# Kernel tuning notes

Measured on AMD Instinct MI355X. Metric: run time of the kernel, lower is better.

## Reference

```python
import jax, jax.numpy as jnp
import numpy as np


def floor_ste(x):
    # forward: floor(x); backward: identity (straight-through estimator)
    return x + jax.lax.stop_gradient(jnp.floor(x) - x)


def _int_polynomial(x_int, sf):
    c0, c1, c2 = 0.35815147, 0.96963238, 1.0
    b_int = floor_ste((c1 / c0) / sf)
    c_int = floor_ste((c2 / c0) / (sf * sf))
    z = x_int * (x_int + b_int) + c_int
    return z, c0 * sf * sf


def _int_exp(x_int, sf):
    x0 = -0.69314718
    n = 15
    x0_int = floor_ste(x0 / sf)
    x_int = jnp.maximum(x_int, n * x0_int)
    q = floor_ste(x_int / x0_int)
    r = x_int - x0_int * q
    exp_int, exp_sf = _int_polynomial(r, sf)
    exp_int = jnp.maximum(floor_ste(exp_int * jnp.exp2(n - q)), 0.0)
    return exp_int, exp_sf / (2.0 ** n)


def _int_softmax(x, sf):
    x_int = x / sf
    x_int = x_int - jnp.max(x_int, axis=-1, keepdims=True)
    exp_int, exp_sf = _int_exp(x_int, sf)
    exp_int_sum = jnp.sum(exp_int, axis=-1, keepdims=True)
    return exp_int, exp_int_sum, exp_sf


def setup_inputs() -> dict:
    key = jax.random.key(0)
    k1, = jax.random.split(key, 1)
    x = jax.random.normal(k1, (2, 16, 1024, 1024), dtype=jnp.float32)
    scale = jnp.float32(0.05)          # activation quantization step
    threshold = jnp.array([0.1], dtype=jnp.float32)  # nn.Parameter init
    return {"x": x, "scale": scale, "threshold": threshold}


def reference(x, scale, threshold):
    output_bit = 8
    threshold_bits = 8
    exp_int, exp_int_sum, exp_sf = _int_softmax(x, scale)
    factor = floor_ste((2.0 ** 32) / exp_int_sum)
    out_scale_A = threshold / (2.0 ** output_bit - 1.0)   # shape [1]
    out_scale_B = 1.0 / (2.0 ** output_bit - 1.0)
    approx_threshold = (floor_ste(threshold * 2.0 ** threshold_bits)
                        * exp_int_sum / (2.0 ** threshold_bits))
    mask_A = exp_int <= approx_threshold
    exp_int_A = jnp.where(mask_A, exp_int, 0.0)
    exp_int_B = jnp.where(mask_A, 0.0, exp_int)
    softmax_int_A = floor_ste(exp_int_A * factor / ((2.0 ** 32) * out_scale_A))
    softmax_int_B = floor_ste(exp_int_B * factor / ((2.0 ** 32) * out_scale_B))
    softmax_int_B = jnp.minimum(softmax_int_B, 255.0)
    return softmax_int_A * out_scale_A + softmax_int_B * out_scale_B
```

## Files before the change

### kernel.cpp

```cpp
#include <hip/hip_runtime.h>
#include <math.h>

#pragma clang fp contract(off)

#define TPB 256
#define ROWLEN 1024

typedef float f32x4 __attribute__((ext_vector_type(4)));

static __device__ __forceinline__ float bcast_f32(float v) {
    return __int_as_float(__builtin_amdgcn_readfirstlane(__float_as_int(v)));
}

__device__ __forceinline__ float wave_max_dpp(float m) {
    const int NI = 0xff800000;
    int v;
    v = __builtin_amdgcn_update_dpp(NI, __float_as_int(m), 0x111, 0xf, 0xf, false);
    m = fmaxf(m, __int_as_float(v));
    v = __builtin_amdgcn_update_dpp(NI, __float_as_int(m), 0x112, 0xf, 0xf, false);
    m = fmaxf(m, __int_as_float(v));
    v = __builtin_amdgcn_update_dpp(NI, __float_as_int(m), 0x114, 0xf, 0xf, false);
    m = fmaxf(m, __int_as_float(v));
    v = __builtin_amdgcn_update_dpp(NI, __float_as_int(m), 0x118, 0xf, 0xf, false);
    m = fmaxf(m, __int_as_float(v));
    v = __builtin_amdgcn_update_dpp(NI, __float_as_int(m), 0x142, 0xa, 0xf, false);
    m = fmaxf(m, __int_as_float(v));
    v = __builtin_amdgcn_update_dpp(NI, __float_as_int(m), 0x143, 0xc, 0xf, false);
    m = fmaxf(m, __int_as_float(v));
    return __int_as_float(__builtin_amdgcn_readlane(__float_as_int(m), 63));
}

__device__ __forceinline__ void wave_sum_dpp2(unsigned& a, unsigned& b) {
    int v0, v1;
#define SSTG(sel, rm, bm) \
    v0 = __builtin_amdgcn_update_dpp(0, (int)a, sel, rm, bm, false); \
    v1 = __builtin_amdgcn_update_dpp(0, (int)b, sel, rm, bm, false); \
    a += (unsigned)v0; b += (unsigned)v1;
    SSTG(0x111,0xf,0xf) SSTG(0x112,0xf,0xf) SSTG(0x114,0xf,0xf)
    SSTG(0x118,0xf,0xf) SSTG(0x142,0xa,0xf) SSTG(0x143,0xc,0xf)
#undef SSTG
    a = (unsigned)__builtin_amdgcn_readlane((int)a, 63);
    b = (unsigned)__builtin_amdgcn_readlane((int)b, 63);
}

__device__ __forceinline__ float fac_exact(double s) {
    const float r0 = __builtin_amdgcn_rcpf((float)s);
    float qf = floorf(4294967296.0f * r0);
    const double t = (double)qf * s;
    if (t > 4294967296.0)           qf -= 1.0f;
    else if (t + s <= 4294967296.0) qf += 1.0f;
    return qf;
}

__global__ __launch_bounds__(TPB, 8) void qsplit_int_softmax_kernel(
    const float* __restrict__ x,
    const float* __restrict__ scale_p,
    const float* __restrict__ thr_p,
    float* __restrict__ out,
    const int rows)
{
    const int tid  = threadIdx.x;
    const int lane = tid & 63;
    const int wid  = tid >> 6;
    const int r    = (int)(blockIdx.x << 2) | wid;
    if (r >= rows) return;

    const float sf  = scale_p[0];
    const float thr = thr_p[0];

    const float rh = bcast_f32(1.0f / sf);
    const float er = __builtin_fmaf(-sf, rh, 1.0f);
    const float rl = bcast_f32(rh * er);

    #define DF_DIV(a) ({ float _p = (a) * rh; \
                         float _e = __builtin_fmaf((a), rh, -_p); \
                         _p + __builtin_fmaf((a), rl, _e); })
    const float x0f    = bcast_f32(floorf(DF_DIV(-0.69314718f)));
    const float bfc    = bcast_f32(floorf(DF_DIV(2.7073824f)));
    const float s2     = sf * sf;
    const float r2h    = 1.0f / s2;
    const float r2e    = __builtin_fmaf(-s2, r2h, 1.0f);
    const float r2l    = r2h * r2e;
    const float cq     = __builtin_fmaf(2.7921141f, r2l,
                         2.7921141f * r2h);
    const float cfc    = bcast_f32(floorf(cq));
    const float clampf = bcast_f32(15.0f * x0f);
    const float invx0f = bcast_f32(1.0f / x0f);

    const float osA  = bcast_f32(thr / 255.0f);
    const float osB  = bcast_f32(1.0f / 255.0f);
    const float invA = bcast_f32(1.0f / (4294967296.0f * osA));
    const float invB = bcast_f32(1.0f / (4294967296.0f * osB));
    const float thrq = bcast_f32(floorf(thr * 256.0f));

    const float* px = x + (size_t)r * ROWLEN + ((size_t)lane << 2);
    float a[16];
    #pragma unroll
    for (int g = 0; g < 4; ++g) {
        const f32x4 v = *(const f32x4*)(px + (g << 8));
        a[4*g+0] = v[0]; a[4*g+1] = v[1];
        a[4*g+2] = v[2]; a[4*g+3] = v[3];
    }

    #pragma unroll
    for (int j = 0; j < 16; ++j) {
        const float xx = a[j];
        const float p  = xx * rh;
        const float e  = __builtin_fmaf(xx, rh, -p);
        a[j] = p + __builtin_fmaf(xx, rl, e);
    }

    float t0 = fmaxf(a[0],a[1]),  t1 = fmaxf(a[2],a[3]);
    float t2 = fmaxf(a[4],a[5]),  t3 = fmaxf(a[6],a[7]);
    float t4 = fmaxf(a[8],a[9]),  t5 = fmaxf(a[10],a[11]);
    float t6 = fmaxf(a[12],a[13]),t7 = fmaxf(a[14],a[15]);
    t0 = fmaxf(t0,t1); t2 = fmaxf(t2,t3); t4 = fmaxf(t4,t5); t6 = fmaxf(t6,t7);
    const float m = wave_max_dpp(fmaxf(fmaxf(t0,t2), fmaxf(t4,t6)));

    unsigned usum = 0;
    #pragma unroll
    for (int j = 0; j < 16; ++j) {
        float v = a[j] - m;
        v = fmaxf(v, clampf);
        const float qf = floorf(v * invx0f);
        const int   qi = (int)qf;
        const float rr = v - x0f * qf;
        const float t  = rr + bfc;
        const float z  = rr * t + cfc;
        float ei = floorf(ldexpf(z, 15 - qi));
        ei = fmaxf(ei, 0.0f);
        a[j] = ei;
        usum += (unsigned)ei;
    }

    unsigned lo = usum & 0xFFFFu, hi = usum >> 16;
    wave_sum_dpp2(lo, hi);
    const double s = (double)(((unsigned long long)hi << 16) + lo);

    const float fac_f = bcast_f32(fac_exact(s));
    const float ath_f = bcast_f32((float)(((double)thrq * s) * (1.0 / 256.0)));

    float* po = out + (size_t)r * ROWLEN + ((size_t)lane << 2);
    #pragma unroll
    for (int g = 0; g < 4; ++g) {
        f32x4 o;
        #pragma unroll
        for (int jj = 0; jj < 4; ++jj) {
            const float ei  = a[4*g+jj];
            const bool  isA = (ei <= ath_f);
            const float t1_ = ei * fac_f;
            const float t2_ = t1_ * (isA ? invA : invB);
            float si = floorf(t2_);
            si = fminf(si, isA ? 3.0e38f : 255.0f);
            o[jj] = si * (isA ? osA : osB);
        }
        __builtin_nontemporal_store(o, (f32x4*)(po + (g << 8)));
    }
}

extern "C" void kernel_launch(void* const* d_in, const int* in_sizes, int n_in,
                              void* d_out, int out_size, void* d_ws, size_t ws_size,
                              hipStream_t stream) {
    const float* x     = (const float*)d_in[0];
    const float* scale = (const float*)d_in[1];
    const float* thr   = (const float*)d_in[2];
    float* out = (float*)d_out;

    const int total = in_sizes[0];
    const int rows  = total / ROWLEN;

    const int blocks = (rows + 3) / 4;

    qsplit_int_softmax_kernel<<<dim3(blocks), dim3(TPB), 0, stream>>>(
        x, scale, thr, out, rows);
}
```

Before: 233.8 us.

## Use persistent waves with LDS double-staging via global_load_lds prefetch

```diff
diff --git a/kernel.cpp b/kernel.cpp
--- a/kernel.cpp
+++ b/kernel.cpp
@@ -5,6 +5,7 @@
 
 #define TPB 256
 #define ROWLEN 1024
+#define BLOCKS 1024
 
 typedef float f32x4 __attribute__((ext_vector_type(4)));
 
@@ -52,7 +53,7 @@
     return qf;
 }
 
-__global__ __launch_bounds__(TPB, 8) void qsplit_int_softmax_kernel(
+__global__ __launch_bounds__(TPB) void qsplit_int_softmax_kernel(
     const float* __restrict__ x,
     const float* __restrict__ scale_p,
     const float* __restrict__ thr_p,
@@ -62,8 +63,15 @@
     const int tid  = threadIdx.x;
     const int lane = tid & 63;
     const int wid  = tid >> 6;
-    const int r    = (int)(blockIdx.x << 2) | wid;
-    if (r >= rows) return;
+
+    __shared__ float lds[4][ROWLEN];
+
+    const int gw = (int)(blockIdx.x << 2) | wid;
+    const int W  = (int)(gridDim.x << 2);
+    const int chunk = (rows + W - 1) / W;
+    int r          = gw * chunk;
+    const int rend = (r + chunk < rows) ? (r + chunk) : rows;
+    if (r >= rend) return;
 
     const float sf  = scale_p[0];
     const float thr = thr_p[0];
@@ -93,69 +101,93 @@
     const float invB = bcast_f32(1.0f / (4294967296.0f * osB));
     const float thrq = bcast_f32(floorf(thr * 256.0f));
 
-    const float* px = x + (size_t)r * ROWLEN + ((size_t)lane << 2);
-    float a[16];
-    #pragma unroll
-    for (int g = 0; g < 4; ++g) {
-        const f32x4 v = *(const f32x4*)(px + (g << 8));
-        a[4*g+0] = v[0]; a[4*g+1] = v[1];
-        a[4*g+2] = v[2]; a[4*g+3] = v[3];
+    #define STAGE(row) do { \
+        const float* _s = x + (size_t)(row) * ROWLEN + ((size_t)lane << 2); \
+        _Pragma("unroll") \
+        for (int _g = 0; _g < 4; ++_g) { \
+            __builtin_amdgcn_global_load_lds( \
+                (const __attribute__((address_space(1))) void*)(_s + (_g << 8)), \
+                (__attribute__((address_space(3))) void*)&lds[wid][_g << 8], \
+                16, 0, 0); \
+        } \
+    } while (0)
+
+    STAGE(r);
+
+    for (; r < rend; ++r) {
+        asm volatile("s_waitcnt vmcnt(0)" ::: "memory");
+
+        f32x4 w0 = *(const f32x4*)&lds[wid][(0 << 8) | (lane << 2)];
+        f32x4 w1 = *(const f32x4*)&lds[wid][(1 << 8) | (lane << 2)];
+        f32x4 w2 = *(const f32x4*)&lds[wid][(2 << 8) | (lane << 2)];
+        f32x4 w3 = *(const f32x4*)&lds[wid][(3 << 8) | (lane << 2)];
+
+        asm volatile("s_waitcnt lgkmcnt(0)" ::: "memory");
+
+        if (r + 1 < rend) STAGE(r + 1);
+
+        float a[16];
+        a[0]=w0[0]; a[1]=w0[1]; a[2]=w0[2]; a[3]=w0[3];
+        a[4]=w1[0]; a[5]=w1[1]; a[6]=w1[2]; a[7]=w1[3];
+        a[8]=w2[0]; a[9]=w2[1]; a[10]=w2[2]; a[11]=w2[3];
+        a[12]=w3[0]; a[13]=w3[1]; a[14]=w3[2]; a[15]=w3[3];
+
+        #pragma unroll
+        for (int j = 0; j < 16; ++j) {
+            const float xx = a[j];
+            const float p  = xx * rh;
+            const float e  = __builtin_fmaf(xx, rh, -p);
+            a[j] = p + __builtin_fmaf(xx, rl, e);
+        }
+
+        float t0 = fmaxf(a[0],a[1]),  t1 = fmaxf(a[2],a[3]);
+        float t2 = fmaxf(a[4],a[5]),  t3 = fmaxf(a[6],a[7]);
+        float t4 = fmaxf(a[8],a[9]),  t5 = fmaxf(a[10],a[11]);
+        float t6 = fmaxf(a[12],a[13]),t7 = fmaxf(a[14],a[15]);
+        t0 = fmaxf(t0,t1); t2 = fmaxf(t2,t3); t4 = fmaxf(t4,t5); t6 = fmaxf(t6,t7);
+        const float m = wave_max_dpp(fmaxf(fmaxf(t0,t2), fmaxf(t4,t6)));
+
+        unsigned usum = 0;
+        #pragma unroll
+        for (int j = 0; j < 16; ++j) {
+            float v = a[j] - m;
+            v = fmaxf(v, clampf);
+            const float qf = floorf(v * invx0f);
+            const int   qi = (int)qf;
+            const float rr = v - x0f * qf;
+            const float t  = rr + bfc;
+            const float z  = rr * t + cfc;
+            float ei = floorf(ldexpf(z, 15 - qi));
+            ei = fmaxf(ei, 0.0f);
+            a[j] = ei;
+            usum += (unsigned)ei;
+        }
+
+        unsigned lo = usum & 0xFFFFu, hi = usum >> 16;
+        wave_sum_dpp2(lo, hi);
+        const double s = (double)(((unsigned long long)hi << 16) + lo);
+
+        const float fac_f = bcast_f32(fac_exact(s));
+        const float ath_f = bcast_f32((float)(((double)thrq * s) * (1.0 / 256.0)));
+
+        float* po = out + (size_t)r * ROWLEN + ((size_t)lane << 2);
+        #pragma unroll
+        for (int g = 0; g < 4; ++g) {
+            f32x4 o;
+            #pragma unroll
+            for (int jj = 0; jj < 4; ++jj) {
+                const float ei  = a[4*g+jj];
+                const bool  isA = (ei <= ath_f);
+                const float t1_ = ei * fac_f;
+                const float t2_ = t1_ * (isA ? invA : invB);
+                float si = floorf(t2_);
+                si = fminf(si, isA ? 3.0e38f : 255.0f);
+                o[jj] = si * (isA ? osA : osB);
+            }
+            __builtin_nontemporal_store(o, (f32x4*)(po + (g << 8)));
+        }
     }
-
-    #pragma unroll
-    for (int j = 0; j < 16; ++j) {
-        const float xx = a[j];
-        const float p  = xx * rh;
-        const float e  = __builtin_fmaf(xx, rh, -p);
-        a[j] = p + __builtin_fmaf(xx, rl, e);
-    }
-
-    float t0 = fmaxf(a[0],a[1]),  t1 = fmaxf(a[2],a[3]);
-    float t2 = fmaxf(a[4],a[5]),  t3 = fmaxf(a[6],a[7]);
-    float t4 = fmaxf(a[8],a[9]),  t5 = fmaxf(a[10],a[11]);
-    float t6 = fmaxf(a[12],a[13]),t7 = fmaxf(a[14],a[15]);
-    t0 = fmaxf(t0,t1); t2 = fmaxf(t2,t3); t4 = fmaxf(t4,t5); t6 = fmaxf(t6,t7);
-    const float m = wave_max_dpp(fmaxf(fmaxf(t0,t2), fmaxf(t4,t6)));
-
-    unsigned usum = 0;
-    #pragma unroll
-    for (int j = 0; j < 16; ++j) {
-        float v = a[j] - m;
-        v = fmaxf(v, clampf);
-        const float qf = floorf(v * invx0f);
-        const int   qi = (int)qf;
-        const float rr = v - x0f * qf;
-        const float t  = rr + bfc;
-        const float z  = rr * t + cfc;
-        float ei = floorf(ldexpf(z, 15 - qi));
-        ei = fmaxf(ei, 0.0f);
-        a[j] = ei;
-        usum += (unsigned)ei;
-    }
-
-    unsigned lo = usum & 0xFFFFu, hi = usum >> 16;
-    wave_sum_dpp2(lo, hi);
-    const double s = (double)(((unsigned long long)hi << 16) + lo);
-
-    const float fac_f = bcast_f32(fac_exact(s));
-    const float ath_f = bcast_f32((float)(((double)thrq * s) * (1.0 / 256.0)));
-
-    float* po = out + (size_t)r * ROWLEN + ((size_t)lane << 2);
-    #pragma unroll
-    for (int g = 0; g < 4; ++g) {
-        f32x4 o;
-        #pragma unroll
-        for (int jj = 0; jj < 4; ++jj) {
-            const float ei  = a[4*g+jj];
-            const bool  isA = (ei <= ath_f);
-            const float t1_ = ei * fac_f;
-            const float t2_ = t1_ * (isA ? invA : invB);
-            float si = floorf(t2_);
-            si = fminf(si, isA ? 3.0e38f : 255.0f);
-            o[jj] = si * (isA ? osA : osB);
-        }
-        __builtin_nontemporal_store(o, (f32x4*)(po + (g << 8)));
-    }
+    #undef STAGE
 }
 
 extern "C" void kernel_launch(void* const* d_in, const int* in_sizes, int n_in,
@@ -169,8 +201,6 @@
     const int total = in_sizes[0];
     const int rows  = total / ROWLEN;
 
-    const int blocks = (rows + 3) / 4;
-
-    qsplit_int_softmax_kernel<<<dim3(blocks), dim3(TPB), 0, stream>>>(
+    qsplit_int_softmax_kernel<<<dim3(BLOCKS), dim3(TPB), 0, stream>>>(
         x, scale, thr, out, rows);
 }
```

New measurement: 237.3 us. Within noise of the previous version (+1.5%).
